# Performance work log

Hardware: AMD Instinct MI355X
Metric: run time of the kernel (lower is better)

Reference implementation:

```python
import jax, jax.numpy as jnp
import numpy as np

NOOBJ_LAMBDA = 0.5
COORD_LAMBDA = 5.0


def _cxcywh_to_xyxy(b):
    cx, cy, w, h = b[..., 0], b[..., 1], b[..., 2], b[..., 3]
    return jnp.stack([cx - w / 2, cy - h / 2, cx + w / 2, cy + h / 2], axis=-1)


def _pairwise_iou(a, b):
    # a: [B, N, 4] xyxy (preds), b: [B, M, 4] xyxy (targets) -> [B, N, M]
    lt = jnp.maximum(a[:, :, None, :2], b[:, None, :, :2])
    rb = jnp.minimum(a[:, :, None, 2:], b[:, None, :, 2:])
    wh = jnp.clip(rb - lt, 0.0)
    inter = wh[..., 0] * wh[..., 1]
    area_a = (a[..., 2] - a[..., 0]) * (a[..., 3] - a[..., 1])
    area_b = (b[..., 2] - b[..., 0]) * (b[..., 3] - b[..., 1])
    union = area_a[:, :, None] + area_b[:, None, :] - inter
    return inter / jnp.where(union > 0, union, 1.0)


def setup_inputs() -> dict:
    key = jax.random.key(0)
    kp, kt, km = jax.random.split(key, 3)
    B = 8192
    # positive values so sqrt(w), sqrt(h) is well-defined (as the torch code assumes)
    pred = jax.random.uniform(kp, (B, 7, 7, 30), dtype=jnp.float32, minval=0.05, maxval=1.0)
    target = jax.random.uniform(kt, (B, 7, 7, 30), dtype=jnp.float32, minval=0.05, maxval=1.0)
    # target confidence channel (index 4) is the obj/noobj indicator: 0 or 1
    obj = (jax.random.uniform(km, (B, 7, 7)) < 0.2).astype(jnp.float32)
    target = target.at[..., 4].set(obj)
    return {"pred_tensor": pred, "target_tensor": target}


def reference(pred_tensor, target_tensor):
    B = pred_tensor.shape[0]
    pred = pred_tensor.reshape(B, 49, 30)
    target = target_tensor.reshape(B, 49, 30)

    conf_t = target[..., 4]            # [B,49]
    noobj = conf_t == 0                # [B,49]
    obj = conf_t > 0                   # [B,49]

    # --- no-object confidence loss (channels 4 and 9) ---
    d4 = pred[..., 4] - target[..., 4]
    d9 = pred[..., 9] - target[..., 9]
    noobj_loss = jnp.sum(jnp.where(noobj, d4 * d4 + d9 * d9, 0.0))

    # --- object cells: 2 boxes per cell, padded to all 49 cells with a mask ---
    pb = pred[..., :10].reshape(B, 98, 5)
    tb = target[..., :10].reshape(B, 98, 5)
    box_mask = jnp.repeat(obj, 2, axis=1)  # [B,98]

    p_xyxy = _cxcywh_to_xyxy(pb[..., :4])
    t_xyxy = _cxcywh_to_xyxy(tb[..., :4])
    iou = _pairwise_iou(p_xyxy, t_xyxy)  # [B,98,98]
    pair_mask = box_mask[:, :, None] & box_mask[:, None, :]
    iou = jnp.where(pair_mask, iou, 0.0)
    max_iou = jnp.max(iou, axis=1)       # max over pred boxes, per target box [B,98]
    cmask = (max_iou != 0) & box_mask    # [B,98]

    cm = cmask.astype(pred.dtype)
    # coord (cx,cy) loss
    dxy = pb[..., :2] - tb[..., :2]
    coord_loss_cxcy = jnp.sum(cm * jnp.sum(dxy * dxy, axis=-1))
    # coord (sqrt w, sqrt h) loss
    dwh = jnp.sqrt(pb[..., 2:4]) - jnp.sqrt(tb[..., 2:4])
    coord_loss_wh = jnp.sum(cm * jnp.sum(dwh * dwh, axis=-1))
    # object confidence loss
    dconf = pb[..., 4] - tb[..., 4]
    obj_loss = jnp.sum(cm * dconf * dconf)

    # --- class loss over object cells ---
    dcls = pred[..., 10:] - target[..., 10:]
    cls_loss = jnp.sum(obj.astype(pred.dtype) * jnp.sum(dcls * dcls, axis=-1))

    bsz = jnp.asarray(B, pred.dtype)
    batch_cls_loss = cls_loss / bsz
    batch_obj_loss = (obj_loss + noobj_loss * NOOBJ_LAMBDA) / bsz
    batch_coord_loss = (coord_loss_cxcy + coord_loss_wh) * COORD_LAMBDA / bsz
    batch_loss = batch_cls_loss + batch_obj_loss + batch_coord_loss
    return (batch_loss, batch_cls_loss, batch_obj_loss, batch_coord_loss)
```

## Files before the change

kernel.cpp:

```cpp
#include <hip/hip_runtime.h>

#define CH 30
#define CELLS 49
#define ROW (CELLS * CH)
#define RPB 4

__device__ __forceinline__ float waveReduce(float v) {
    #pragma unroll
    for (int o = 32; o > 0; o >>= 1) v += __shfl_xor(v, o, 64);
    return v;
}

__global__ __launch_bounds__(256) void yolo_main(const float* __restrict__ pred,
                                                 const float* __restrict__ targ,
                                                 float* __restrict__ ws,
                                                 int B, int NB) {
    const int w = threadIdx.x >> 6;
    const int lane = threadIdx.x & 63;
    const int r = blockIdx.x * RPB + w;

    __shared__ float4 boxS[RPB][98];
    __shared__ int clist[RPB][49];
    __shared__ float partial[RPB][3];

    const float* P = pred + (size_t)r * ROW;
    const float* T = targ + (size_t)r * ROW;
    const bool act = (lane < CELLS) && (r < B);

    float cls = 0.f, objc = 0.f, coord = 0.f;
    bool isObj = false;

    if (act) {
        const int cb = lane * CH;
        const float t4 = T[cb + 4];
        const float p4 = P[cb + 4];
        const float p9 = P[cb + 9];
        const float t9 = T[cb + 9];
        isObj = t4 > 0.f;
        if (!isObj) {
            const float d9 = p9 - t9;
            objc = 0.5f * (p4 * p4 + d9 * d9);
        } else {
            const float2* pc = (const float2*)(P + cb + 10);
            const float2* tc = (const float2*)(T + cb + 10);
            #pragma unroll
            for (int k = 0; k < 10; ++k) {
                const float2 a = pc[k], b2 = tc[k];
                const float dx = a.x - b2.x, dy = a.y - b2.y;
                cls += dx * dx + dy * dy;
            }
        }
    }

    const unsigned long long m = __ballot(isObj);
    const int nObj = __popcll(m);
    if (isObj) {
        const int pos = __popcll(m & ((1ull << lane) - 1ull));
        clist[w][pos] = lane;
    }
    __syncthreads();

    const int nBox = 2 * nObj;

    for (int e = lane; e < nBox; e += 64) {
        const int c = clist[w][e >> 1];
        const float* pb = P + c * CH + (e & 1) * 5;
        const float cx = pb[0], cy = pb[1], bw = pb[2], bh = pb[3];
        boxS[w][e] = make_float4(cx - 0.5f * bw, cy - 0.5f * bh,
                                 cx + 0.5f * bw, cy + 0.5f * bh);
    }
    __syncthreads();

    for (int e = lane; e < nBox; e += 64) {
        const int c = clist[w][e >> 1];
        const int bb = c * CH + (e & 1) * 5;
        const float tcx = T[bb], tcy = T[bb + 1], tw = T[bb + 2], th = T[bb + 3];
        const float tx1 = tcx - 0.5f * tw, ty1 = tcy - 0.5f * th;
        const float tx2 = tcx + 0.5f * tw, ty2 = tcy + 0.5f * th;
        const float ta = (tx2 - tx1) * (ty2 - ty1);
        float maxiou = 0.f;
        for (int i = 0; i < nBox; ++i) {
            const float4 pb4 = boxS[w][i];
            const float lx = fmaxf(pb4.x, tx1), ly = fmaxf(pb4.y, ty1);
            const float rx = fminf(pb4.z, tx2), ry = fminf(pb4.w, ty2);
            const float iw = fmaxf(rx - lx, 0.f), ih = fmaxf(ry - ly, 0.f);
            const float inter = iw * ih;
            const float pa = (pb4.z - pb4.x) * (pb4.w - pb4.y);
            const float un = pa + ta - inter;
            const float iou = inter / (un > 0.f ? un : 1.f);
            maxiou = fmaxf(maxiou, iou);
        }
        if (maxiou != 0.f) {
            const float dcx = P[bb] - tcx, dcy = P[bb + 1] - tcy;
            coord += dcx * dcx + dcy * dcy;
            const float dw = sqrtf(P[bb + 2]) - sqrtf(tw);
            const float dh = sqrtf(P[bb + 3]) - sqrtf(th);
            coord += dw * dw + dh * dh;
            const float dc = P[bb + 4] - T[bb + 4];
            objc += dc * dc;
        }
    }

    cls = waveReduce(cls); objc = waveReduce(objc); coord = waveReduce(coord);
    if (lane == 0) { partial[w][0] = cls; partial[w][1] = objc; partial[w][2] = coord; }
    __syncthreads();
    if (threadIdx.x == 0) {
        float c = 0.f, o = 0.f, x = 0.f;
        #pragma unroll
        for (int i = 0; i < RPB; ++i) { c += partial[i][0]; o += partial[i][1]; x += partial[i][2]; }
        ws[blockIdx.x] = c;
        ws[NB + blockIdx.x] = o;
        ws[2 * NB + blockIdx.x] = x;
    }
}

__global__ __launch_bounds__(1024) void yolo_reduce(const float* __restrict__ ws,
                                                    float* __restrict__ out,
                                                    int NB, float invB) {
    const int tid = threadIdx.x;
    const int w = tid >> 6, lane = tid & 63;
    __shared__ float sred[16];
    __shared__ float sums[3];
    #pragma unroll
    for (int s = 0; s < 3; ++s) {
        float v = 0.f;
        for (int i = tid; i < NB; i += 1024) v += ws[s * NB + i];
        v = waveReduce(v);
        if (lane == 0) sred[w] = v;
        __syncthreads();
        if (tid == 0) {
            float t = 0.f;
            #pragma unroll
            for (int k = 0; k < 16; ++k) t += sred[k];
            sums[s] = t;
        }
        __syncthreads();
    }
    if (tid == 0) {
        const float bcls = sums[0] * invB;
        const float bobj = sums[1] * invB;
        const float bcoord = sums[2] * 5.0f * invB;
        out[0] = bcls + bobj + bcoord;
        out[1] = bcls;
        out[2] = bobj;
        out[3] = bcoord;
    }
}

extern "C" void kernel_launch(void* const* d_in, const int* in_sizes, int n_in,
                              void* d_out, int out_size, void* d_ws, size_t ws_size,
                              hipStream_t stream) {
    const float* pred = (const float*)d_in[0];
    const float* targ = (const float*)d_in[1];
    float* ws = (float*)d_ws;
    float* out = (float*)d_out;
    const int B = in_sizes[0] / ROW;
    const int NB = (B + RPB - 1) / RPB;

    yolo_main<<<NB, 256, 0, stream>>>(pred, targ, ws, B, NB);
    yolo_reduce<<<1, 1024, 0, stream>>>(ws, out, NB, 1.0f / (float)B);
}
```

Baseline: 126.0 us.

## Stream rows with coalesced float2 loads and stage box channels in LDS

```diff
diff --git a/kernel.cpp b/kernel.cpp
--- a/kernel.cpp
+++ b/kernel.cpp
@@ -18,45 +18,50 @@
     const int w = threadIdx.x >> 6;
     const int lane = threadIdx.x & 63;
     const int r = blockIdx.x * RPB + w;
+    const bool rowOk = (r < B);
 
-    __shared__ float4 boxS[RPB][98];
-    __shared__ int clist[RPB][49];
+    __shared__ float spb[RPB][CELLS * 10];
+    __shared__ float stb[RPB][CELLS * 10];
+    __shared__ float4 boxS[RPB][2 * CELLS];
+    __shared__ int clist[RPB][CELLS];
     __shared__ float partial[RPB][3];
 
     const float* P = pred + (size_t)r * ROW;
     const float* T = targ + (size_t)r * ROW;
-    const bool act = (lane < CELLS) && (r < B);
+
+    bool isObj = false;
+    if (rowOk && lane < CELLS) isObj = T[lane * CH + 4] > 0.f;
+    const unsigned long long mask = __ballot(isObj);
+    const int nObj = __popcll(mask);
+    if (isObj) {
+        const int pos = __popcll(mask & ((1ull << lane) - 1ull));
+        clist[w][pos] = lane;
+    }
 
     float cls = 0.f, objc = 0.f, coord = 0.f;
-    bool isObj = false;
 
-    if (act) {
-        const int cb = lane * CH;
-        const float t4 = T[cb + 4];
-        const float p4 = P[cb + 4];
-        const float p9 = P[cb + 9];
-        const float t9 = T[cb + 9];
-        isObj = t4 > 0.f;
-        if (!isObj) {
-            const float d9 = p9 - t9;
-            objc = 0.5f * (p4 * p4 + d9 * d9);
-        } else {
-            const float2* pc = (const float2*)(P + cb + 10);
-            const float2* tc = (const float2*)(T + cb + 10);
-            #pragma unroll
-            for (int k = 0; k < 10; ++k) {
-                const float2 a = pc[k], b2 = tc[k];
-                const float dx = a.x - b2.x, dy = a.y - b2.y;
-                cls += dx * dx + dy * dy;
+    if (rowOk) {
+        const float2* P2 = (const float2*)P;
+        const float2* T2 = (const float2*)T;
+        for (int j = lane; j < ROW / 2; j += 64) {
+            const float2 p = P2[j];
+            const float2 t = T2[j];
+            const int cell = j / 15;
+            const int ch0 = 2 * (j - cell * 15);
+            const bool obj = (mask >> cell) & 1ull;
+            if (ch0 >= 10) {
+                if (obj) {
+                    const float dx = p.x - t.x, dy = p.y - t.y;
+                    cls += dx * dx + dy * dy;
+                }
+            } else if (obj) {
+                *(float2*)&spb[w][cell * 10 + ch0] = p;
+                *(float2*)&stb[w][cell * 10 + ch0] = t;
+            } else {
+                if (ch0 == 4) objc += 0.5f * p.x * p.x;
+                else if (ch0 == 8) { const float d = p.y - t.y; objc += 0.5f * d * d; }
             }
         }
-    }
-
-    const unsigned long long m = __ballot(isObj);
-    const int nObj = __popcll(m);
-    if (isObj) {
-        const int pos = __popcll(m & ((1ull << lane) - 1ull));
-        clist[w][pos] = lane;
     }
     __syncthreads();
 
@@ -64,7 +69,7 @@
 
     for (int e = lane; e < nBox; e += 64) {
         const int c = clist[w][e >> 1];
-        const float* pb = P + c * CH + (e & 1) * 5;
+        const float* pb = &spb[w][c * 10 + (e & 1) * 5];
         const float cx = pb[0], cy = pb[1], bw = pb[2], bh = pb[3];
         boxS[w][e] = make_float4(cx - 0.5f * bw, cy - 0.5f * bh,
                                  cx + 0.5f * bw, cy + 0.5f * bh);
@@ -73,8 +78,9 @@
 
     for (int e = lane; e < nBox; e += 64) {
         const int c = clist[w][e >> 1];
-        const int bb = c * CH + (e & 1) * 5;
-        const float tcx = T[bb], tcy = T[bb + 1], tw = T[bb + 2], th = T[bb + 3];
+        const int bb = c * 10 + (e & 1) * 5;
+        const float tcx = stb[w][bb], tcy = stb[w][bb + 1];
+        const float tw = stb[w][bb + 2], th = stb[w][bb + 3];
         const float tx1 = tcx - 0.5f * tw, ty1 = tcy - 0.5f * th;
         const float tx2 = tcx + 0.5f * tw, ty2 = tcy + 0.5f * th;
         const float ta = (tx2 - tx1) * (ty2 - ty1);
@@ -91,12 +97,12 @@
             maxiou = fmaxf(maxiou, iou);
         }
         if (maxiou != 0.f) {
-            const float dcx = P[bb] - tcx, dcy = P[bb + 1] - tcy;
+            const float dcx = spb[w][bb] - tcx, dcy = spb[w][bb + 1] - tcy;
             coord += dcx * dcx + dcy * dcy;
-            const float dw = sqrtf(P[bb + 2]) - sqrtf(tw);
-            const float dh = sqrtf(P[bb + 3]) - sqrtf(th);
+            const float dw = sqrtf(spb[w][bb + 2]) - sqrtf(tw);
+            const float dh = sqrtf(spb[w][bb + 3]) - sqrtf(th);
             coord += dw * dw + dh * dh;
-            const float dc = P[bb + 4] - T[bb + 4];
+            const float dc = spb[w][bb + 4] - stb[w][bb + 4];
             objc += dc * dc;
         }
     }
```

Result: slower. 133.2 us (+5.7%).
